# Optimization experiments

Hardware: AMD Instinct MI355X
Metric: run time of the kernel (lower is better)

The kernel has to match this reference:

```python
import jax, jax.numpy as jnp
import numpy as np

N_NODES = 100000
N_EDGES = 3200000
D_FEAT = 128
N_CLASSES = 40


def setup_inputs() -> dict:
    key = jax.random.key(0)
    k1, k2, k3, k4 = jax.random.split(key, 4)
    x = jax.random.normal(k1, (N_NODES, D_FEAT), dtype=jnp.float32)
    edge_index = jax.random.randint(k2, (2, N_EDGES), 0, N_NODES, dtype=jnp.int64)
    # torch.nn.Linear default init ~ U(-1/sqrt(fan_in), 1/sqrt(fan_in)); randn is fine for a numeric baseline
    W = jax.random.normal(k3, (N_CLASSES, D_FEAT), dtype=jnp.float32) * (1.0 / np.sqrt(D_FEAT))
    b = jax.random.normal(k4, (N_CLASSES,), dtype=jnp.float32) * 0.01
    return {"x": x, "edge_index": edge_index, "W": W, "b": b, "K": 2}


def _sgc_forward(x, edge_index, W, b, K):
    N = x.shape[0]
    loop = jnp.arange(N, dtype=edge_index.dtype)
    # Outer add_self_loops in SGC.forward, then gcn_norm inside SGConv adds
    # self-loops AGAIN (PyG default add_self_loops=True) -> two self-loops per node.
    row = jnp.concatenate([edge_index[0], loop, loop])
    col = jnp.concatenate([edge_index[1], loop, loop])
    # gcn_norm: deg over destination (col) with unit edge weights
    deg = jax.ops.segment_sum(jnp.ones_like(row, dtype=x.dtype), col, num_segments=N)
    dinv = jnp.where(deg > 0, deg ** -0.5, 0.0)
    norm = dinv[row] * dinv[col]  # [E+2N]
    for _ in range(K):
        # out[col] += norm * x[row]  (K-hop symmetric-normalized propagation)
        x = jax.ops.segment_sum(norm[:, None] * x[row], col, num_segments=N)
    logits = x @ W.T + b  # [N, C]
    return jax.nn.log_softmax(logits, axis=1)


def reference(x, edge_index, W, b, K):
    return _sgc_forward(x, edge_index, W, b, K)
```

## Files before the change

kernel.cpp:

```cpp
#include <hip/hip_runtime.h>
#include <hip/hip_bf16.h>
#include <math.h>

#define DF 128
#define NC 40
#define GST 40
#define RB 8
#define RSZ 256
#define CHUNK 4096
#define CAP 12288

__device__ __forceinline__ float bf2f(unsigned short h) {
  unsigned int u = ((unsigned int)h) << 16;
  union { unsigned int u; float f; } c; c.u = u; return c.f;
}
__device__ __forceinline__ unsigned short f2bf(float x) {
  union { float f; unsigned int u; } c; c.f = x;
  unsigned int u = c.u;
  return (unsigned short)((u + 0x7fffu + ((u >> 16) & 1u)) >> 16);
}

__global__ __launch_bounds__(512) void k_binB(
    const int* __restrict__ row, const int* __restrict__ col,
    int* __restrict__ cnt, unsigned int* __restrict__ slab, int E, int NB) {
  __shared__ int colS[CHUNK];
  __shared__ int hist[512];
  __shared__ int cursor[512];
  int t = threadIdx.x;
  if (t < NB) hist[t] = 0;
  int s = blockIdx.x * CHUNK, e = min(E, s + CHUNK), n = e - s;
  for (int i = t; i < n; i += 512) colS[i] = col[s + i];
  __syncthreads();
  for (int i = t; i < n; i += 512) atomicAdd(&hist[colS[i] >> RB], 1);
  __syncthreads();
  if (t < NB) cursor[t] = hist[t] ? atomicAdd(&cnt[t], hist[t]) : 0;
  __syncthreads();
  for (int i = t; i < n; i += 512) {
    int c = colS[i];
    int b = c >> RB;
    int p = atomicAdd(&cursor[b], 1);
    slab[(size_t)b * CAP + p] = ((unsigned int)row[s + i] << RB) | (unsigned int)(c & (RSZ - 1));
  }
}

__global__ __launch_bounds__(512) void k_bucket_scan(
    const int* __restrict__ cnt, int* __restrict__ base,
    int* __restrict__ off, int NB, int N, int E) {
  __shared__ int s[512];
  int t = threadIdx.x;
  int v = (t < NB) ? cnt[t] : 0;
  s[t] = v;
  __syncthreads();
  for (int o = 1; o < 512; o <<= 1) {
    int u = (t >= o) ? s[t - o] : 0;
    __syncthreads();
    s[t] += u;
    __syncthreads();
  }
  if (t < NB) base[t] = s[t] - v;
  if (t == 0) { base[NB] = E; off[N] = E; }
}

__global__ __launch_bounds__(512) void k_binC(
    const unsigned int* __restrict__ slab, const int* __restrict__ base,
    int* __restrict__ off, int* __restrict__ eidx, float* __restrict__ dinv, int N) {
  __shared__ int hist[RSZ];
  __shared__ int sc[RSZ];
  __shared__ int cur[RSZ];
  int b = blockIdx.x;
  int t = threadIdx.x;
  if (t < RSZ) hist[t] = 0;
  __syncthreads();
  int cb = base[b], ce = base[b + 1];
  int cnt_b = ce - cb;
  const unsigned int* src = slab + (size_t)b * CAP;
  for (int i = t; i < cnt_b; i += 512) atomicAdd(&hist[src[i] & (RSZ - 1)], 1);
  __syncthreads();
  int v = (t < RSZ) ? hist[t] : 0;
  if (t < RSZ) sc[t] = v;
  __syncthreads();
  for (int o = 1; o < RSZ; o <<= 1) {
    int u = (t < RSZ && t >= o) ? sc[t - o] : 0;
    __syncthreads();
    if (t < RSZ) sc[t] += u;
    __syncthreads();
  }
  if (t < RSZ) {
    int pos = cb + sc[t] - v;
    int node = (b << RB) + t;
    if (node < N) {
      off[node] = pos;
      dinv[node] = rsqrtf((float)v + 2.0f);
    }
    cur[t] = pos;
  }
  __syncthreads();
  for (int i = t; i < cnt_b; i += 512) {
    unsigned int en = src[i];
    int p = atomicAdd(&cur[en & (RSZ - 1)], 1);
    eidx[p] = (int)(en >> RB);
  }
}

__global__ __launch_bounds__(128) void k_xw_scale(
    const float* __restrict__ x, const float* __restrict__ W,
    const float* __restrict__ dinv, unsigned short* __restrict__ g0, int N) {
  __shared__ float4 Ws[NC * (DF / 4)];
  for (int i = threadIdx.x; i < NC * (DF / 4); i += blockDim.x)
    Ws[i] = ((const float4*)W)[i];
  __syncthreads();
  int node = blockIdx.x * blockDim.x + threadIdx.x;
  if (node >= N) return;
  float acc[NC];
#pragma unroll
  for (int c = 0; c < NC; ++c) acc[c] = 0.f;
  const float4* xr = (const float4*)(x + (size_t)node * DF);
#pragma unroll 1
  for (int ch = 0; ch < 8; ++ch) {
    float4 v0 = xr[ch * 4 + 0];
    float4 v1 = xr[ch * 4 + 1];
    float4 v2 = xr[ch * 4 + 2];
    float4 v3 = xr[ch * 4 + 3];
#pragma unroll
    for (int c = 0; c < NC; ++c) {
      float4 w0 = Ws[c * (DF / 4) + ch * 4 + 0];
      float4 w1 = Ws[c * (DF / 4) + ch * 4 + 1];
      float4 w2 = Ws[c * (DF / 4) + ch * 4 + 2];
      float4 w3 = Ws[c * (DF / 4) + ch * 4 + 3];
      acc[c] += (v0.x * w0.x + v0.y * w0.y + v0.z * w0.z + v0.w * w0.w) +
                (v1.x * w1.x + v1.y * w1.y + v1.z * w1.z + v1.w * w1.w) +
                (v2.x * w2.x + v2.y * w2.y + v2.z * w2.z + v2.w * w2.w) +
                (v3.x * w3.x + v3.y * w3.y + v3.z * w3.z + v3.w * w3.w);
    }
  }
  float di = dinv[node];
  unsigned int pk[NC / 2];
#pragma unroll
  for (int c2 = 0; c2 < NC / 2; ++c2) {
    unsigned int lo = f2bf(di * acc[c2 * 2 + 0]);
    unsigned int hi = f2bf(di * acc[c2 * 2 + 1]);
    pk[c2] = lo | (hi << 16);
  }
  uint4* gp = (uint4*)(g0 + (size_t)node * GST);
#pragma unroll
  for (int q = 0; q < 5; ++q)
    gp[q] = make_uint4(pk[q * 4 + 0], pk[q * 4 + 1], pk[q * 4 + 2], pk[q * 4 + 3]);
}

#define GATHER16                                                        \
    int r0 = eidx[i + 0], r1 = eidx[i + 1], r2 = eidx[i + 2], r3 = eidx[i + 3];   \
    int r4 = eidx[i + 4], r5 = eidx[i + 5], r6 = eidx[i + 6], r7 = eidx[i + 7];   \
    int r8 = eidx[i + 8], r9 = eidx[i + 9], rA = eidx[i + 10], rB = eidx[i + 11]; \
    int rC = eidx[i + 12], rD = eidx[i + 13], rE = eidx[i + 14], rF = eidx[i + 15]; \
    unsigned short a0 = gl[(size_t)r0 * GST]; unsigned short a1 = gl[(size_t)r1 * GST]; \
    unsigned short a2 = gl[(size_t)r2 * GST]; unsigned short a3 = gl[(size_t)r3 * GST]; \
    unsigned short a4 = gl[(size_t)r4 * GST]; unsigned short a5 = gl[(size_t)r5 * GST]; \
    unsigned short a6 = gl[(size_t)r6 * GST]; unsigned short a7 = gl[(size_t)r7 * GST]; \
    unsigned short a8 = gl[(size_t)r8 * GST]; unsigned short a9 = gl[(size_t)r9 * GST]; \
    unsigned short aA = gl[(size_t)rA * GST]; unsigned short aB = gl[(size_t)rB * GST]; \
    unsigned short aC = gl[(size_t)rC * GST]; unsigned short aD = gl[(size_t)rD * GST]; \
    unsigned short aE = gl[(size_t)rE * GST]; unsigned short aF = gl[(size_t)rF * GST]; \
    acc += (((bf2f(a0) + bf2f(a1)) + (bf2f(a2) + bf2f(a3))) +           \
            ((bf2f(a4) + bf2f(a5)) + (bf2f(a6) + bf2f(a7)))) +          \
           (((bf2f(a8) + bf2f(a9)) + (bf2f(aA) + bf2f(aB))) +           \
            ((bf2f(aC) + bf2f(aD)) + (bf2f(aE) + bf2f(aF))));

__global__ __launch_bounds__(256) void k_hop_mid(
    const int* __restrict__ off, const int* __restrict__ eidx,
    const float* __restrict__ dinv, const unsigned short* __restrict__ gin,
    unsigned short* __restrict__ gout, int N) {
  int wave = (int)((blockIdx.x * (size_t)blockDim.x + threadIdx.x) >> 6);
  int lane = threadIdx.x & 63;
  if (wave >= N) return;
  int node = wave;
  int s = __builtin_amdgcn_readfirstlane(off[node]);
  int e = __builtin_amdgcn_readfirstlane(off[node + 1]);
  if (lane < NC) {
    const unsigned short* gl = gin + lane;
    float acc = 2.0f * bf2f(gl[(size_t)node * GST]);
    int i = s;
    for (; i + 16 <= e; i += 16) { GATHER16 }
    for (; i + 4 <= e; i += 4) {
      int r0 = eidx[i + 0], r1 = eidx[i + 1], r2 = eidx[i + 2], r3 = eidx[i + 3];
      unsigned short a0 = gl[(size_t)r0 * GST];
      unsigned short a1 = gl[(size_t)r1 * GST];
      unsigned short a2 = gl[(size_t)r2 * GST];
      unsigned short a3 = gl[(size_t)r3 * GST];
      acc += (bf2f(a0) + bf2f(a1)) + (bf2f(a2) + bf2f(a3));
    }
    for (; i < e; ++i) acc += bf2f(gl[(size_t)eidx[i] * GST]);
    float di = dinv[node];
    gout[(size_t)node * GST + lane] = f2bf(di * di * acc);
  }
}

__global__ __launch_bounds__(256) void k_hop_final(
    const int* __restrict__ off, const int* __restrict__ eidx,
    const float* __restrict__ dinv, const unsigned short* __restrict__ gin,
    const float* __restrict__ bias, float* __restrict__ out, int N) {
  int wave = (int)((blockIdx.x * (size_t)blockDim.x + threadIdx.x) >> 6);
  int lane = threadIdx.x & 63;
  if (wave >= N) return;
  int node = wave;
  int s = __builtin_amdgcn_readfirstlane(off[node]);
  int e = __builtin_amdgcn_readfirstlane(off[node + 1]);
  float acc = 0.f;
  bool act = lane < NC;
  if (act) {
    const unsigned short* gl = gin + lane;
    acc = 2.0f * bf2f(gl[(size_t)node * GST]);
    int i = s;
    for (; i + 16 <= e; i += 16) { GATHER16 }
    for (; i + 4 <= e; i += 4) {
      int r0 = eidx[i + 0], r1 = eidx[i + 1], r2 = eidx[i + 2], r3 = eidx[i + 3];
      unsigned short a0 = gl[(size_t)r0 * GST];
      unsigned short a1 = gl[(size_t)r1 * GST];
      unsigned short a2 = gl[(size_t)r2 * GST];
      unsigned short a3 = gl[(size_t)r3 * GST];
      acc += (bf2f(a0) + bf2f(a1)) + (bf2f(a2) + bf2f(a3));
    }
    for (; i < e; ++i) acc += bf2f(gl[(size_t)eidx[i] * GST]);
  }
  float di = dinv[node];
  float v = act ? (di * acc + bias[lane]) : -3.0e38f;
  float m = v;
#pragma unroll
  for (int o = 32; o > 0; o >>= 1) m = fmaxf(m, __shfl_xor(m, o, 64));
  float ex = act ? expf(v - m) : 0.f;
  float ssum = ex;
#pragma unroll
  for (int o = 32; o > 0; o >>= 1) ssum += __shfl_xor(ssum, o, 64);
  float lse = m + logf(ssum);
  if (act) out[(size_t)node * NC + lane] = v - lse;
}

extern "C" void kernel_launch(void* const* d_in, const int* in_sizes, int n_in,
                              void* d_out, int out_size, void* d_ws, size_t ws_size,
                              hipStream_t stream) {
  const float* x = (const float*)d_in[0];
  const int* ei  = (const int*)d_in[1];
  const float* W = (const float*)d_in[2];
  const float* b = (const float*)d_in[3];
  float* out = (float*)d_out;

  const int N = in_sizes[0] / DF;
  const int E = in_sizes[1] / 2;
  const int NB = (N + RSZ - 1) >> RB;
  const int* row  = ei;
  const int* colv = ei + E;

  char* basep = (char*)d_ws;
  auto alloc = [&](size_t bytes) {
    char* p = basep;
    basep += (bytes + 511) & ~(size_t)511;
    return p;
  };
  int*   cnt    = (int*)  alloc(((size_t)NB) * 4);
  int*   bbase  = (int*)  alloc(((size_t)NB + 1) * 4);
  unsigned int* slab = (unsigned int*)alloc((size_t)NB * CAP * 4);
  int*   off    = (int*)  alloc(((size_t)N + 1) * 4);
  int*   eidx   = (int*)  alloc((size_t)E * 4);
  float* dinv   = (float*)alloc((size_t)N * 4);
  unsigned short* g0 = (unsigned short*)alloc((size_t)N * GST * 2);
  unsigned short* g1 = (unsigned short*)alloc((size_t)N * GST * 2);

  const int B = 256;
  const int gBin = (E + CHUNK - 1) / CHUNK;

  hipMemsetAsync(cnt, 0, (size_t)NB * 4, stream);
  k_binB<<<gBin, 512, 0, stream>>>(row, colv, cnt, slab, E, NB);
  k_bucket_scan<<<1, 512, 0, stream>>>(cnt, bbase, off, NB, N, E);
  k_binC<<<NB, 512, 0, stream>>>(slab, bbase, off, eidx, dinv, N);

  k_xw_scale<<<(N + 127) / 128, 128, 0, stream>>>(x, W, dinv, g0, N);

  const int gWave = (int)(((size_t)N * 64 + B - 1) / B);
  k_hop_mid  <<<gWave, B, 0, stream>>>(off, eidx, dinv, g0, g1, N);
  k_hop_final<<<gWave, B, 0, stream>>>(off, eidx, dinv, g1, b, out, N);
}
```

Before: 336.1 us.

## Split propagated features into two half-planes and gather 12 edges per wave

The bf16 projected features are split into two planes of 20 classes each, stored as 5 uint2 per node. Each hop kernel processes one half-plane per block, with lanes arranged as 12 edge slots by 5 chunks, and combines partial sums with shuffles. The goal is wider 8-byte loads and higher gather parallelism per wave, with each half-plane small enough to stay cache-resident. The trade-off is that log-softmax now runs in a separate kernel, with logits written to and re-read from the slab workspace. Nontemporal loads and stores are added for the edge indices and outputs.

```diff
diff --git a/kernel.cpp b/kernel.cpp
--- a/kernel.cpp
+++ b/kernel.cpp
@@ -4,12 +4,14 @@
 
 #define DF 128
 #define NC 40
-#define GST 40
+#define PC 20
 #define RB 8
 #define RSZ 256
 #define CHUNK 4096
 #define CAP 12288
 
+typedef float f32x4 __attribute__((ext_vector_type(4)));
+
 __device__ __forceinline__ float bf2f(unsigned short h) {
   unsigned int u = ((unsigned int)h) << 16;
   union { unsigned int u; float f; } c; c.u = u; return c.f;
@@ -18,6 +20,12 @@
   union { float f; unsigned int u; } c; c.f = x;
   unsigned int u = c.u;
   return (unsigned short)((u + 0x7fffu + ((u >> 16) & 1u)) >> 16);
+}
+__device__ __forceinline__ float blo(unsigned int u) {
+  union { unsigned int u; float f; } c; c.u = u << 16; return c.f;
+}
+__device__ __forceinline__ float bhi(unsigned int u) {
+  union { unsigned int u; float f; } c; c.u = u & 0xffff0000u; return c.f;
 }
 
 __global__ __launch_bounds__(512) void k_binB(
@@ -141,88 +149,91 @@
     unsigned int hi = f2bf(di * acc[c2 * 2 + 1]);
     pk[c2] = lo | (hi << 16);
   }
-  uint4* gp = (uint4*)(g0 + (size_t)node * GST);
-#pragma unroll
-  for (int q = 0; q < 5; ++q)
-    gp[q] = make_uint4(pk[q * 4 + 0], pk[q * 4 + 1], pk[q * 4 + 2], pk[q * 4 + 3]);
-}
-
-#define GATHER16                                                        \
-    int r0 = eidx[i + 0], r1 = eidx[i + 1], r2 = eidx[i + 2], r3 = eidx[i + 3];   \
-    int r4 = eidx[i + 4], r5 = eidx[i + 5], r6 = eidx[i + 6], r7 = eidx[i + 7];   \
-    int r8 = eidx[i + 8], r9 = eidx[i + 9], rA = eidx[i + 10], rB = eidx[i + 11]; \
-    int rC = eidx[i + 12], rD = eidx[i + 13], rE = eidx[i + 14], rF = eidx[i + 15]; \
-    unsigned short a0 = gl[(size_t)r0 * GST]; unsigned short a1 = gl[(size_t)r1 * GST]; \
-    unsigned short a2 = gl[(size_t)r2 * GST]; unsigned short a3 = gl[(size_t)r3 * GST]; \
-    unsigned short a4 = gl[(size_t)r4 * GST]; unsigned short a5 = gl[(size_t)r5 * GST]; \
-    unsigned short a6 = gl[(size_t)r6 * GST]; unsigned short a7 = gl[(size_t)r7 * GST]; \
-    unsigned short a8 = gl[(size_t)r8 * GST]; unsigned short a9 = gl[(size_t)r9 * GST]; \
-    unsigned short aA = gl[(size_t)rA * GST]; unsigned short aB = gl[(size_t)rB * GST]; \
-    unsigned short aC = gl[(size_t)rC * GST]; unsigned short aD = gl[(size_t)rD * GST]; \
-    unsigned short aE = gl[(size_t)rE * GST]; unsigned short aF = gl[(size_t)rF * GST]; \
-    acc += (((bf2f(a0) + bf2f(a1)) + (bf2f(a2) + bf2f(a3))) +           \
-            ((bf2f(a4) + bf2f(a5)) + (bf2f(a6) + bf2f(a7)))) +          \
-           (((bf2f(a8) + bf2f(a9)) + (bf2f(aA) + bf2f(aB))) +           \
-            ((bf2f(aC) + bf2f(aD)) + (bf2f(aE) + bf2f(aF))));
-
-__global__ __launch_bounds__(256) void k_hop_mid(
+  uint2* p0 = (uint2*)g0 + (size_t)node * 5;
+  uint2* p1 = (uint2*)g0 + (size_t)N * 5 + (size_t)node * 5;
+#pragma unroll
+  for (int q = 0; q < 5; ++q) {
+    p0[q] = make_uint2(pk[2 * q], pk[2 * q + 1]);
+    p1[q] = make_uint2(pk[10 + 2 * q], pk[10 + 2 * q + 1]);
+  }
+}
+
+template<int FINAL>
+__global__ __launch_bounds__(256) void k_hop(
     const int* __restrict__ off, const int* __restrict__ eidx,
     const float* __restrict__ dinv, const unsigned short* __restrict__ gin,
-    unsigned short* __restrict__ gout, int N) {
+    unsigned short* __restrict__ gout, float* __restrict__ logits,
+    const float* __restrict__ bias, int N, int NBH) {
+  int bid = blockIdx.x;
+  int slot8 = bid & 7;
+  int half = slot8 >> 2;
+  int nbi = ((bid >> 3) << 2) + (slot8 & 3);
+  if (nbi >= NBH) return;
+  int lane = threadIdx.x & 63;
+  int node = (nbi << 2) + (threadIdx.x >> 6);
+  if (node >= N) return;
+  int slot = lane / 5;
+  unsigned j = (unsigned)(lane - slot * 5);
+  const uint2* plane = (const uint2*)gin + (size_t)half * ((size_t)N * 5);
+  int s = __builtin_amdgcn_readfirstlane(off[node]);
+  int e = __builtin_amdgcn_readfirstlane(off[node + 1]);
+  float a0 = 0.f, a1 = 0.f, a2 = 0.f, a3 = 0.f;
+  unsigned selfoff = (unsigned)node * 5u + j;
+  if (slot == 0) {
+    uint2 v = plane[selfoff];
+    a0 = 2.f * blo(v.x); a1 = 2.f * bhi(v.x);
+    a2 = 2.f * blo(v.y); a3 = 2.f * bhi(v.y);
+  }
+  int i = s;
+  if (slot < 12) {
+    for (; i + 12 <= e; i += 12) {
+      int r = __builtin_nontemporal_load(eidx + i + slot);
+      uint2 v = plane[(unsigned)r * 5u + j];
+      a0 += blo(v.x); a1 += bhi(v.x); a2 += blo(v.y); a3 += bhi(v.y);
+    }
+    if (slot < e - i) {
+      int r = __builtin_nontemporal_load(eidx + i + slot);
+      uint2 v = plane[(unsigned)r * 5u + j];
+      a0 += blo(v.x); a1 += bhi(v.x); a2 += blo(v.y); a3 += bhi(v.y);
+    }
+  }
+  int l30 = (lane + 30) & 63, l15 = (lane + 15) & 63;
+  a0 += __shfl(a0, l30, 64); a1 += __shfl(a1, l30, 64);
+  a2 += __shfl(a2, l30, 64); a3 += __shfl(a3, l30, 64);
+  a0 += __shfl(a0, l15, 64); a1 += __shfl(a1, l15, 64);
+  a2 += __shfl(a2, l15, 64); a3 += __shfl(a3, l15, 64);
+  int l5 = (lane + 5) & 63, l10 = (lane + 10) & 63;
+  a0 = a0 + __shfl(a0, l5, 64) + __shfl(a0, l10, 64);
+  a1 = a1 + __shfl(a1, l5, 64) + __shfl(a1, l10, 64);
+  a2 = a2 + __shfl(a2, l5, 64) + __shfl(a2, l10, 64);
+  a3 = a3 + __shfl(a3, l5, 64) + __shfl(a3, l10, 64);
+  if (slot == 0) {
+    float di = dinv[node];
+    if (FINAL) {
+      float4 bb = ((const float4*)bias)[half * 5 + (int)j];
+      f32x4 lg = { di * a0 + bb.x, di * a1 + bb.y,
+                   di * a2 + bb.z, di * a3 + bb.w };
+      f32x4* dst = (f32x4*)(logits + (size_t)node * NC + half * PC + 4u * j);
+      __builtin_nontemporal_store(lg, dst);
+    } else {
+      float sc = di * di;
+      unsigned lo = (unsigned)f2bf(sc * a0) | ((unsigned)f2bf(sc * a1) << 16);
+      unsigned hi = (unsigned)f2bf(sc * a2) | ((unsigned)f2bf(sc * a3) << 16);
+      unsigned long long pk = (unsigned long long)lo | ((unsigned long long)hi << 32);
+      unsigned long long* dst =
+          (unsigned long long*)((uint2*)gout + (size_t)half * ((size_t)N * 5) + selfoff);
+      __builtin_nontemporal_store(pk, dst);
+    }
+  }
+}
+
+__global__ __launch_bounds__(256) void k_lsm(
+    const float* __restrict__ logits, float* __restrict__ out, int N) {
   int wave = (int)((blockIdx.x * (size_t)blockDim.x + threadIdx.x) >> 6);
   int lane = threadIdx.x & 63;
   if (wave >= N) return;
-  int node = wave;
-  int s = __builtin_amdgcn_readfirstlane(off[node]);
-  int e = __builtin_amdgcn_readfirstlane(off[node + 1]);
-  if (lane < NC) {
-    const unsigned short* gl = gin + lane;
-    float acc = 2.0f * bf2f(gl[(size_t)node * GST]);
-    int i = s;
-    for (; i + 16 <= e; i += 16) { GATHER16 }
-    for (; i + 4 <= e; i += 4) {
-      int r0 = eidx[i + 0], r1 = eidx[i + 1], r2 = eidx[i + 2], r3 = eidx[i + 3];
-      unsigned short a0 = gl[(size_t)r0 * GST];
-      unsigned short a1 = gl[(size_t)r1 * GST];
-      unsigned short a2 = gl[(size_t)r2 * GST];
-      unsigned short a3 = gl[(size_t)r3 * GST];
-      acc += (bf2f(a0) + bf2f(a1)) + (bf2f(a2) + bf2f(a3));
-    }
-    for (; i < e; ++i) acc += bf2f(gl[(size_t)eidx[i] * GST]);
-    float di = dinv[node];
-    gout[(size_t)node * GST + lane] = f2bf(di * di * acc);
-  }
-}
-
-__global__ __launch_bounds__(256) void k_hop_final(
-    const int* __restrict__ off, const int* __restrict__ eidx,
-    const float* __restrict__ dinv, const unsigned short* __restrict__ gin,
-    const float* __restrict__ bias, float* __restrict__ out, int N) {
-  int wave = (int)((blockIdx.x * (size_t)blockDim.x + threadIdx.x) >> 6);
-  int lane = threadIdx.x & 63;
-  if (wave >= N) return;
-  int node = wave;
-  int s = __builtin_amdgcn_readfirstlane(off[node]);
-  int e = __builtin_amdgcn_readfirstlane(off[node + 1]);
-  float acc = 0.f;
   bool act = lane < NC;
-  if (act) {
-    const unsigned short* gl = gin + lane;
-    acc = 2.0f * bf2f(gl[(size_t)node * GST]);
-    int i = s;
-    for (; i + 16 <= e; i += 16) { GATHER16 }
-    for (; i + 4 <= e; i += 4) {
-      int r0 = eidx[i + 0], r1 = eidx[i + 1], r2 = eidx[i + 2], r3 = eidx[i + 3];
-      unsigned short a0 = gl[(size_t)r0 * GST];
-      unsigned short a1 = gl[(size_t)r1 * GST];
-      unsigned short a2 = gl[(size_t)r2 * GST];
-      unsigned short a3 = gl[(size_t)r3 * GST];
-      acc += (bf2f(a0) + bf2f(a1)) + (bf2f(a2) + bf2f(a3));
-    }
-    for (; i < e; ++i) acc += bf2f(gl[(size_t)eidx[i] * GST]);
-  }
-  float di = dinv[node];
-  float v = act ? (di * acc + bias[lane]) : -3.0e38f;
+  float v = act ? __builtin_nontemporal_load(logits + (size_t)wave * NC + lane) : -3.0e38f;
   float m = v;
 #pragma unroll
   for (int o = 32; o > 0; o >>= 1) m = fmaxf(m, __shfl_xor(m, o, 64));
@@ -231,7 +242,7 @@
 #pragma unroll
   for (int o = 32; o > 0; o >>= 1) ssum += __shfl_xor(ssum, o, 64);
   float lse = m + logf(ssum);
-  if (act) out[(size_t)node * NC + lane] = v - lse;
+  if (act) __builtin_nontemporal_store(v - lse, out + (size_t)wave * NC + lane);
 }
 
 extern "C" void kernel_launch(void* const* d_in, const int* in_sizes, int n_in,
@@ -261,10 +272,10 @@
   int*   off    = (int*)  alloc(((size_t)N + 1) * 4);
   int*   eidx   = (int*)  alloc((size_t)E * 4);
   float* dinv   = (float*)alloc((size_t)N * 4);
-  unsigned short* g0 = (unsigned short*)alloc((size_t)N * GST * 2);
-  unsigned short* g1 = (unsigned short*)alloc((size_t)N * GST * 2);
-
-  const int B = 256;
+  unsigned short* g0 = (unsigned short*)alloc((size_t)N * NC * 2);
+  unsigned short* g1 = (unsigned short*)alloc((size_t)N * NC * 2);
+  float* logits = (float*)slab;
+
   const int gBin = (E + CHUNK - 1) / CHUNK;
 
   hipMemsetAsync(cnt, 0, (size_t)NB * 4, stream);
@@ -274,7 +285,12 @@
 
   k_xw_scale<<<(N + 127) / 128, 128, 0, stream>>>(x, W, dinv, g0, N);
 
-  const int gWave = (int)(((size_t)N * 64 + B - 1) / B);
-  k_hop_mid  <<<gWave, B, 0, stream>>>(off, eidx, dinv, g0, g1, N);
-  k_hop_final<<<gWave, B, 0, stream>>>(off, eidx, dinv, g1, b, out, N);
-}
+  const int NBH = (N + 3) >> 2;
+  const int NBH4 = (NBH + 3) & ~3;
+  const int gHop = 2 * NBH4;
+  k_hop<0><<<gHop, 256, 0, stream>>>(off, eidx, dinv, g0, g1, nullptr, nullptr, N, NBH);
+  k_hop<1><<<gHop, 256, 0, stream>>>(off, eidx, dinv, g1, nullptr, logits, b, N, NBH);
+
+  const int gLsm = (int)(((size_t)N * 64 + 255) / 256);
+  k_lsm<<<gLsm, 256, 0, stream>>>(logits, out, N);
+}
```

Result: slower. 448.1 us (+33.3%).
